# Kernel optimization log

Hardware: AMD Instinct MI355X
Metric: run time of the kernel (lower is better)

## Reference

```python
import jax, jax.numpy as jnp
import numpy as np

B, C, D, T = 64, 512, 32, 32
DT = D * T
K = 128            # valid_num: top-K proposals kept for NMS-style pooling
MARGIN = 0.2       # opt.global_margin
MAX_VIOLATION = True
EPS = 1e-8         # torch.cosine_similarity eps


def _l2n(x, axis):
    # torch cosine_similarity normalizes each vector by max(||x||, eps)
    return x / jnp.maximum(jnp.linalg.norm(x, axis=axis, keepdims=True), EPS)


def _cos(a, b, axis):
    return jnp.sum(_l2n(a, axis) * _l2n(b, axis), axis=axis)


def setup_inputs() -> dict:
    key = jax.random.key(0)
    k1, k2, k3 = jax.random.split(key, 3)
    videos = jax.random.normal(k1, (B, C, D, T), jnp.float32)
    sentences = jax.random.normal(k2, (B, C), jnp.float32)
    iou = jax.random.uniform(k3, (DT, DT), jnp.float32)
    iou_maps = 0.5 * (iou + iou.T)
    iou_maps = iou_maps.at[jnp.arange(DT), jnp.arange(DT)].set(1.0)
    mask = jnp.ones((D, T), jnp.float32)
    lam = jnp.asarray(0.125, jnp.float32)
    return {"videos": videos, "sentences": sentences, "lam": lam,
            "mask": mask, "valid_num": K, "iou_maps": iou_maps}


def reference(videos, sentences, lam, mask, valid_num, iou_maps):
    b, c, d, t = videos.shape
    dt = d * t
    # center over channel dim (dim=1 in torch)
    V = videos - jnp.mean(videos, axis=1, keepdims=True)          # [b,c,d,t]
    S = sentences - jnp.mean(sentences, axis=1, keepdims=True)    # [b,c]
    Vf = V.reshape(b, c, dt)
    Vn = _l2n(Vf, axis=1)                                         # unit over c
    Sn = _l2n(S, axis=1)
    mflat = mask.reshape(dt)

    # cosine sim of every sentence vs every video proposal: [b_sent, b_vid, dt]
    cross = jnp.einsum('ic,jcp->ijp', Sn, Vn)
    cross = jnp.where(mflat == 0, -jnp.inf, cross)

    # --- per-sample positive pooling (loop 1) ---
    self_score = cross[jnp.arange(b), jnp.arange(b)]              # [b, dt]
    w = jax.nn.softmax(self_score, axis=-1)
    video_pos = jnp.einsum('bp,bcp->bc', w, Vf)                   # [b, c]

    # sentence-sentence sims + hard negative mining
    sim = Sn @ Sn.T                                               # [b, b]
    idx = jnp.argsort(-sim, axis=1)                               # descending
    neg_idx = idx[:, 6:b - 5]                                     # b > 11 path
    neg_sents = S[neg_idx]                                        # [b, b-11, c]
    pos_score = _cos(video_pos, S, axis=1)                        # [b]
    neg_score = _cos(video_pos[:, None, :], neg_sents, axis=2)    # [b, b-11]
    vas_loss = jnp.mean(jax.nn.relu(MARGIN + neg_score - pos_score[:, None]), axis=1).mean()

    # cross-video pseudo-positive (crov), gated on nearest-neighbor sim > 0.9
    nn_idx = idx[:, 1]
    pse = Vf[nn_idx]                                              # [b, c, dt]
    vsim = jax.nn.softmax(_cos(video_pos[:, :, None], pse, axis=1), axis=-1)  # [b, dt]
    p_v = jnp.einsum('bp,bcp->bc', vsim, pse)
    n_v = jnp.einsum('bp,bcp->bc', (1.0 - vsim) * mflat, pse) / (valid_num - 1)
    crov = jax.nn.relu(MARGIN + _cos(video_pos, n_v, axis=1) - _cos(video_pos, p_v, axis=1))
    gate = sim[jnp.arange(b), nn_idx] > 0.9
    crov_loss = jnp.where(gate, crov, 0.0).mean()

    # --- NMS-weighted video score pooling (loop 2) ---
    pmap = self_score.reshape(b, d, t)                            # postive_map
    topv, topi = jax.lax.top_k(cross, valid_num)                  # [b,b,K]
    # pairwise IoU among the top-K proposals of each (sentence, video) pair
    iou = iou_maps[topi[..., :, None], topi[..., None, :]]        # [b,b,K,K]
    lower = jnp.tril(jnp.ones((valid_num, valid_num), bool), -1)  # l < k
    decay = jnp.prod(1.0 - jnp.where(lower, iou, 0.0), axis=-1)   # [b,b,K]
    wk = jax.nn.softmax(lam * topv, axis=-1)
    scores = jnp.sum(wk * decay * topv, axis=-1)                  # [b,b]

    # bidirectional margin ranking loss
    diag = jnp.diag(scores)[:, None]
    eye = jnp.eye(b, dtype=bool)
    cost_s = jnp.where(eye, 0.0, jax.nn.relu(MARGIN + scores - diag))
    cost_im = jnp.where(eye, 0.0, jax.nn.relu(MARGIN + scores - diag.T))
    if MAX_VIOLATION:
        cost_s = cost_s.max(axis=1)
        cost_im = cost_im.max(axis=0)
    loss = cost_s.sum() / b + cost_im.sum() / b + vas_loss + crov_loss
    return loss, pmap
```

## Files before the change

### kernel.cpp

```cpp
#include <hip/hip_runtime.h>
#include <hip/hip_fp16.h>
#include <math.h>

#define BB 64
#define CC 512
#define DTT 1024
#define NNEG 53
#define MARGIN_ 0.2f
#define EPSV 1e-8f
#define LDB 132

typedef short s16x8 __attribute__((ext_vector_type(8)));
typedef float f32x4 __attribute__((ext_vector_type(4)));

__device__ __forceinline__ float bred_sum(float v, float* red, int tid, int nt) {
  red[tid] = v; __syncthreads();
  for (int s = nt >> 1; s > 0; s >>= 1) { if (tid < s) red[tid] += red[tid + s]; __syncthreads(); }
  float r = red[0]; __syncthreads();
  return r;
}
__device__ __forceinline__ float bred_max(float v, float* red, int tid, int nt) {
  red[tid] = v; __syncthreads();
  for (int s = nt >> 1; s > 0; s >>= 1) { if (tid < s) red[tid] = fmaxf(red[tid], red[tid + s]); __syncthreads(); }
  float r = red[0]; __syncthreads();
  return r;
}

__global__ void k_sent(const float* __restrict__ sent, float* __restrict__ Sn,
                       float* __restrict__ SnT,
                       unsigned short* __restrict__ SnH, unsigned short* __restrict__ SnL,
                       float* __restrict__ SnSum) {
  int b = blockIdx.x, tid = threadIdx.x;
  __shared__ float red[256];
  float x0 = sent[b * CC + tid], x1 = sent[b * CC + tid + 256];
  float mean = bred_sum(x0 + x1, red, tid, 256) * (1.0f / CC);
  float s0 = x0 - mean, s1 = x1 - mean;
  float ss = bred_sum(s0 * s0 + s1 * s1, red, tid, 256);
  float nrm = fmaxf(sqrtf(ss), EPSV);
  float n0 = s0 / nrm, n1 = s1 / nrm;
  Sn[b * CC + tid] = n0; Sn[b * CC + tid + 256] = n1;
  SnT[tid * BB + b] = n0; SnT[(tid + 256) * BB + b] = n1;
  unsigned u0 = __float_as_uint(n0), u1 = __float_as_uint(n1);
  SnH[b * CC + tid] = (unsigned short)(u0 >> 16);
  SnH[b * CC + tid + 256] = (unsigned short)(u1 >> 16);
  float l0 = n0 - __uint_as_float(u0 & 0xFFFF0000u);
  float l1 = n1 - __uint_as_float(u1 & 0xFFFF0000u);
  SnL[b * CC + tid] = (unsigned short)(__float_as_uint(l0) >> 16);
  SnL[b * CC + tid + 256] = (unsigned short)(__float_as_uint(l1) >> 16);
  float sn = bred_sum(n0 + n1, red, tid, 256);
  if (tid == 0) SnSum[b] = sn;
}

__global__ void k_sim(const float* __restrict__ Sn, const float* __restrict__ SnT,
                      int* __restrict__ nn_idx, int* __restrict__ negidx,
                      float* __restrict__ nnsim) {
  int i = blockIdx.x, tid = threadIdx.x;
  int j = tid & 63, cq = tid >> 6;
  __shared__ float part[4][68];
  __shared__ float srow[BB];
  float acc = 0.f;
  const float* si = Sn + i * CC + cq * 128;
  const float* st = SnT + (size_t)(cq * 128) * BB + j;
#pragma unroll 8
  for (int c = 0; c < 128; ++c) acc = fmaf(si[c], st[(size_t)c * BB], acc);
  part[cq][j] = acc;
  __syncthreads();
  if (tid < 64) srow[tid] = part[0][tid] + part[1][tid] + part[2][tid] + part[3][tid];
  __syncthreads();
  if (tid < 64) {
    float mv = srow[tid];
    int rank = 0;
    for (int k = 0; k < BB; ++k) {
      float vk = srow[k];
      if (vk > mv || (vk == mv && k < tid)) rank++;
    }
    if (rank == 1) { nn_idx[i] = tid; nnsim[i] = mv; }
    if (rank >= 6 && rank < 59) negidx[i * NNEG + rank - 6] = tid;
  }
}

__global__ void k_prep_iou(const float* __restrict__ iou, __half* __restrict__ L16) {
  int g = (blockIdx.x * 256 + threadIdx.x) * 4;
  float4 x = *(const float4*)(iou + g);
  __half2 h0 = __floats2half2_rn(1.f - x.x, 1.f - x.y);
  __half2 h1 = __floats2half2_rn(1.f - x.z, 1.f - x.w);
  *(__half2*)(L16 + g) = h0;
  *(__half2*)(L16 + g + 2) = h1;
}

__global__ __launch_bounds__(256) void k_cross(const float* __restrict__ videos,
    const unsigned short* __restrict__ SnH, const unsigned short* __restrict__ SnL,
    const float* __restrict__ SnSum, const float* __restrict__ mask,
    float* __restrict__ cross, float* __restrict__ meanv, float* __restrict__ normv) {
  __shared__ unsigned int BH[2][16][LDB];
  __shared__ unsigned int BL[2][16][LDB];
  __shared__ float SnSum_s[64];
  __shared__ float mb_s[128];
  __shared__ float inv_s[128];

  int tid = threadIdx.x;
  int j = blockIdx.x >> 3;
  int p0 = (blockIdx.x & 7) << 7;
  int lane = tid & 63;
  int wv = tid >> 6;
  int row = lane & 15;
  int g = lane >> 4;
  int g8 = g << 3;
  int pA = wv << 5;

  int kp = tid >> 4;
  int pb = (tid & 15) << 3;

  const float* vbase = videos + ((size_t)j * CC) * DTT + p0;

  f32x4 acc[4][2];
#pragma unroll
  for (int a = 0; a < 4; ++a)
#pragma unroll
    for (int pf = 0; pf < 2; ++pf)
#pragma unroll
      for (int r = 0; r < 4; ++r) acc[a][pf][r] = 0.f;

  float sacc[8], ssacc[8];
#pragma unroll
  for (int q = 0; q < 8; ++q) { sacc[q] = 0.f; ssacc[q] = 0.f; }

  const float* pr = vbase + (size_t)(2 * kp) * DTT + pb;
  float4 f0 = *(const float4*)(pr);
  float4 f1 = *(const float4*)(pr + 4);
  float4 f2 = *(const float4*)(pr + DTT);
  float4 f3 = *(const float4*)(pr + DTT + 4);

#pragma unroll
  for (int t = 0; t < 16; ++t) {
    int kc = t * 32;
    int cb = t & 1;
    s16x8 AH[4], AL[4];
#pragma unroll
    for (int a = 0; a < 4; ++a) {
      int off = (a * 16 + row) * CC + kc + g8;
      AH[a] = *(const s16x8*)(SnH + off);
      AL[a] = *(const s16x8*)(SnL + off);
    }
    {
      float xe[8] = {f0.x, f0.y, f0.z, f0.w, f1.x, f1.y, f1.z, f1.w};
      float xo[8] = {f2.x, f2.y, f2.z, f2.w, f3.x, f3.y, f3.z, f3.w};
      unsigned int hw[8], lw[8];
#pragma unroll
      for (int q = 0; q < 8; ++q) {
        unsigned ue = __float_as_uint(xe[q]);
        unsigned uo = __float_as_uint(xo[q]);
        hw[q] = (ue >> 16) | (uo & 0xFFFF0000u);
        float el = xe[q] - __uint_as_float(ue & 0xFFFF0000u);
        float ol = xo[q] - __uint_as_float(uo & 0xFFFF0000u);
        lw[q] = (__float_as_uint(el) >> 16) | (__float_as_uint(ol) & 0xFFFF0000u);
        sacc[q] += xe[q] + xo[q];
        ssacc[q] = fmaf(xe[q], xe[q], ssacc[q]);
        ssacc[q] = fmaf(xo[q], xo[q], ssacc[q]);
      }
      *(uint4*)&BH[cb][kp][pb]     = make_uint4(hw[0], hw[1], hw[2], hw[3]);
      *(uint4*)&BH[cb][kp][pb + 4] = make_uint4(hw[4], hw[5], hw[6], hw[7]);
      *(uint4*)&BL[cb][kp][pb]     = make_uint4(lw[0], lw[1], lw[2], lw[3]);
      *(uint4*)&BL[cb][kp][pb + 4] = make_uint4(lw[4], lw[5], lw[6], lw[7]);
    }
    __syncthreads();
    if (t + 1 < 16) {
      const float* pn = vbase + (size_t)((t + 1) * 32 + 2 * kp) * DTT + pb;
      f0 = *(const float4*)(pn);
      f1 = *(const float4*)(pn + 4);
      f2 = *(const float4*)(pn + DTT);
      f3 = *(const float4*)(pn + DTT + 4);
    }
#pragma unroll
    for (int pf = 0; pf < 2; ++pf) {
      int p = pA + pf * 16 + row;
      int kpb = g << 2;
      union { unsigned int u[4]; s16x8 v; } bh, bl;
      bh.u[0] = BH[cb][kpb][p]; bh.u[1] = BH[cb][kpb + 1][p];
      bh.u[2] = BH[cb][kpb + 2][p]; bh.u[3] = BH[cb][kpb + 3][p];
      bl.u[0] = BL[cb][kpb][p]; bl.u[1] = BL[cb][kpb + 1][p];
      bl.u[2] = BL[cb][kpb + 2][p]; bl.u[3] = BL[cb][kpb + 3][p];
#pragma unroll
      for (int a = 0; a < 4; ++a) {
        acc[a][pf] = __builtin_amdgcn_mfma_f32_16x16x32_bf16(AH[a], bh.v, acc[a][pf], 0, 0, 0);
        acc[a][pf] = __builtin_amdgcn_mfma_f32_16x16x32_bf16(AH[a], bl.v, acc[a][pf], 0, 0, 0);
        acc[a][pf] = __builtin_amdgcn_mfma_f32_16x16x32_bf16(AL[a], bh.v, acc[a][pf], 0, 0, 0);
      }
    }
  }

  float (*Sred)[LDB] = (float(*)[LDB])&BH[0][0][0];
  float (*SSred)[LDB] = (float(*)[LDB])&BL[0][0][0];
#pragma unroll
  for (int q = 0; q < 8; ++q) { Sred[kp][pb + q] = sacc[q]; SSred[kp][pb + q] = ssacc[q]; }
  if (tid < 64) SnSum_s[tid] = SnSum[tid];
  __syncthreads();
  if (tid < 128) {
    float s = 0.f, ss = 0.f;
#pragma unroll
    for (int k = 0; k < 16; ++k) { s += Sred[k][tid]; ss += SSred[k][tid]; }
    float mb = s * (1.0f / CC);
    float var = ss - s * mb;
    float nrm = fmaxf(sqrtf(fmaxf(var, 0.f)), EPSV);
    meanv[j * DTT + p0 + tid] = mb;
    normv[j * DTT + p0 + tid] = nrm;
    mb_s[tid] = mb;
    inv_s[tid] = 1.f / nrm;
  }
  __syncthreads();

#pragma unroll
  for (int pf = 0; pf < 2; ++pf) {
    int p = pA + pf * 16 + row;
    float mb = mb_s[p], inv = inv_s[p];
    float mk = mask[p0 + p];
#pragma unroll
    for (int a = 0; a < 4; ++a) {
#pragma unroll
      for (int r = 0; r < 4; ++r) {
        int i = a * 16 + (g << 2) + r;
        float val = (acc[a][pf][r] - mb * SnSum_s[i]) * inv;
        if (mk == 0.f) val = -INFINITY;
        cross[((size_t)i * BB + j) * DTT + p0 + p] = val;
      }
    }
  }
}

__global__ void k_softmax_w(const float* __restrict__ cross, const float* __restrict__ meanv,
                            float* __restrict__ pmap, float* __restrict__ w, float* __restrict__ wm) {
  int b = blockIdx.x, tid = threadIdx.x;
  __shared__ float red[256];
  const float* row = cross + ((size_t)b * BB + b) * DTT;
  float v[4]; float mx = -INFINITY;
#pragma unroll
  for (int q = 0; q < 4; ++q) {
    v[q] = row[q * 256 + tid];
    pmap[b * DTT + q * 256 + tid] = v[q];
    mx = fmaxf(mx, v[q]);
  }
  mx = bred_max(mx, red, tid, 256);
  float e[4]; float se = 0.f;
#pragma unroll
  for (int q = 0; q < 4; ++q) { e[q] = expf(v[q] - mx); se += e[q]; }
  se = bred_sum(se, red, tid, 256);
  float inv = 1.f / se;
  float wmacc = 0.f;
#pragma unroll
  for (int q = 0; q < 4; ++q) {
    float wv = e[q] * inv;
    w[b * DTT + q * 256 + tid] = wv;
    wmacc += wv * meanv[b * DTT + q * 256 + tid];
  }
  wmacc = bred_sum(wmacc, red, tid, 256);
  if (tid == 0) wm[b] = wmacc;
}

__global__ void k_vpos(const float* __restrict__ videos, const float* __restrict__ w,
                       const float* __restrict__ wm, float* __restrict__ vp) {
  int wid = (blockIdx.x * 256 + threadIdx.x) >> 6;
  int lane = threadIdx.x & 63;
  int b = wid >> 9, c = wid & 511;
  const float4* vb = (const float4*)(videos + (size_t)(b * CC + c) * DTT) + lane * 4;
  const float4* wb = (const float4*)(w + b * DTT) + lane * 4;
  float acc = 0.f;
#pragma unroll
  for (int q = 0; q < 4; ++q) {
    float4 x = vb[q], y = wb[q];
    acc += x.x * y.x + x.y * y.y + x.z * y.z + x.w * y.w;
  }
#pragma unroll
  for (int off = 32; off > 0; off >>= 1) acc += __shfl_xor(acc, off);
  if (lane == 0) vp[b * CC + c] = acc - wm[b];
}

__global__ void k_vpnorm(const float* __restrict__ vp, float* __restrict__ vpn,
                         float* __restrict__ vpsum) {
  int b = blockIdx.x, tid = threadIdx.x;
  __shared__ float red[256];
  float x0 = vp[b * CC + tid], x1 = vp[b * CC + tid + 256];
  float ss = bred_sum(x0 * x0 + x1 * x1, red, tid, 256);
  float sm = bred_sum(x0 + x1, red, tid, 256);
  if (tid == 0) { vpn[b] = fmaxf(sqrtf(ss), EPSV); vpsum[b] = sm; }
}

__global__ void k_vsim_logits(const float* __restrict__ videos, const float* __restrict__ vp,
    const float* __restrict__ vpn, const float* __restrict__ vpsum, const int* __restrict__ nn_idx,
    const float* __restrict__ meanv, const float* __restrict__ normv, float* __restrict__ vslog) {
  int gid = blockIdx.x * 256 + threadIdx.x;
  int b = gid >> 10, p = gid & 1023;
  int nn = nn_idx[b];
  const float* base = videos + (size_t)nn * CC * DTT + p;
  const float* vpr = vp + b * CC;
  float acc = 0.f;
#pragma unroll 1
  for (int c0 = 0; c0 < CC; c0 += 16) {
    float v[16];
#pragma unroll
    for (int u = 0; u < 16; ++u) v[u] = base[(size_t)(c0 + u) * DTT];
#pragma unroll
    for (int u = 0; u < 16; ++u) acc = fmaf(vpr[c0 + u], v[u], acc);
  }
  acc -= meanv[nn * DTT + p] * vpsum[b];
  vslog[gid] = acc / (vpn[b] * normv[nn * DTT + p]);
}

__global__ void k_softmax_vsim(float* __restrict__ vslog, const int* __restrict__ nn_idx,
    const float* __restrict__ meanv, const float* __restrict__ mask,
    float* __restrict__ svp, float* __restrict__ svn) {
  int b = blockIdx.x, tid = threadIdx.x;
  __shared__ float red[256];
  int nn = nn_idx[b];
  float v[4]; float mx = -INFINITY;
#pragma unroll
  for (int q = 0; q < 4; ++q) { v[q] = vslog[b * DTT + q * 256 + tid]; mx = fmaxf(mx, v[q]); }
  mx = bred_max(mx, red, tid, 256);
  float e[4]; float se = 0.f;
#pragma unroll
  for (int q = 0; q < 4; ++q) { e[q] = expf(v[q] - mx); se += e[q]; }
  se = bred_sum(se, red, tid, 256);
  float inv = 1.f / se;
  float sp = 0.f, sn2 = 0.f;
#pragma unroll
  for (int q = 0; q < 4; ++q) {
    int p = q * 256 + tid;
    float vs = e[q] * inv;
    vslog[b * DTT + p] = vs;
    float mm = meanv[nn * DTT + p];
    sp += vs * mm;
    sn2 += (1.f - vs) * mask[p] * mm;
  }
  sp = bred_sum(sp, red, tid, 256);
  sn2 = bred_sum(sn2, red, tid, 256);
  if (tid == 0) { svp[b] = sp; svn[b] = sn2; }
}

__global__ void k_pvnv(const float* __restrict__ videos, const float* __restrict__ vsim,
    const int* __restrict__ nn_idx, const float* __restrict__ mask,
    const float* __restrict__ svp, const float* __restrict__ svn, const int* __restrict__ vn_p,
    float* __restrict__ pv, float* __restrict__ nv) {
  int wid = (blockIdx.x * 256 + threadIdx.x) >> 6;
  int lane = threadIdx.x & 63;
  int b = wid >> 9, c = wid & 511;
  int nn = nn_idx[b];
  const float4* vb = (const float4*)(videos + (size_t)(nn * CC + c) * DTT) + lane * 4;
  const float4* vs4 = (const float4*)(vsim + b * DTT) + lane * 4;
  const float4* m4 = ((const float4*)mask) + lane * 4;
  float ap = 0.f, an = 0.f;
#pragma unroll
  for (int q = 0; q < 4; ++q) {
    float4 x = vb[q], s = vs4[q], m = m4[q];
    ap += x.x * s.x + x.y * s.y + x.z * s.z + x.w * s.w;
    an += x.x * (1.f - s.x) * m.x + x.y * (1.f - s.y) * m.y + x.z * (1.f - s.z) * m.z + x.w * (1.f - s.w) * m.w;
  }
#pragma unroll
  for (int off = 32; off > 0; off >>= 1) { ap += __shfl_xor(ap, off); an += __shfl_xor(an, off); }
  if (lane == 0) {
    float kd = (float)(*vn_p - 1);
    pv[b * CC + c] = ap - svp[b];
    nv[b * CC + c] = (an - svn[b]) / kd;
  }
}

__global__ void k_vas(const float* __restrict__ vp, const float* __restrict__ vpn,
                      const float* __restrict__ SnT, const int* __restrict__ negidx,
                      float* __restrict__ vasrow) {
  int i = blockIdx.x, tid = threadIdx.x;
  int t = tid & 63, cq = tid >> 6;
  __shared__ float part[4][68];
  __shared__ float redv[64];
  __shared__ float red[256];
  int nj = (t < NNEG) ? negidx[i * NNEG + t] : i;
  float acc = 0.f;
  const float* vpr = vp + i * CC + cq * 128;
  const float* st = SnT + (size_t)(cq * 128) * BB + nj;
#pragma unroll 8
  for (int c = 0; c < 128; ++c) acc = fmaf(vpr[c], st[(size_t)c * BB], acc);
  part[cq][t] = acc;
  __syncthreads();
  if (tid < 64) redv[tid] = part[0][tid] + part[1][tid] + part[2][tid] + part[3][tid];
  __syncthreads();
  float invn = 1.f / vpn[i];
  float pos = redv[63] * invn;
  float contrib = (tid < NNEG) ? fmaxf(MARGIN_ + redv[tid] * invn - pos, 0.f) : 0.f;
  float s = bred_sum(contrib, red, tid, 256);
  if (tid == 0) vasrow[i] = s / (float)NNEG;
}

__global__ void k_crov(const float* __restrict__ vp, const float* __restrict__ vpn,
                       const float* __restrict__ pv, const float* __restrict__ nv,
                       const float* __restrict__ nnsim, float* __restrict__ crovrow) {
  int b = blockIdx.x, tid = threadIdx.x;
  __shared__ float red[256];
  float dp = 0.f, pp = 0.f, dn = 0.f, nn2 = 0.f;
  for (int c = tid; c < CC; c += 256) {
    float a = vp[b * CC + c], x = pv[b * CC + c], y = nv[b * CC + c];
    dp += a * x; pp += x * x; dn += a * y; nn2 += y * y;
  }
  dp = bred_sum(dp, red, tid, 256);
  pp = bred_sum(pp, red, tid, 256);
  dn = bred_sum(dn, red, tid, 256);
  nn2 = bred_sum(nn2, red, tid, 256);
  if (tid == 0) {
    float cosp = dp / (vpn[b] * fmaxf(sqrtf(pp), EPSV));
    float cosn = dn / (vpn[b] * fmaxf(sqrtf(nn2), EPSV));
    float crov = fmaxf(MARGIN_ + cosn - cosp, 0.f);
    crovrow[b] = (nnsim[b] > 0.9f) ? crov : 0.f;
  }
}

__global__ __launch_bounds__(256) void k_select(const float* __restrict__ cross,
    const int* __restrict__ vn_p, unsigned* __restrict__ ordi_g, float* __restrict__ ordv_g) {
  __shared__ unsigned int hist_s[4][256];
  __shared__ unsigned int sel_s[4][128];
  __shared__ unsigned int selk_s[4][128];
  __shared__ unsigned int cnt_s[4];
  int tid = threadIdx.x;
  int wv = tid >> 6, lane = tid & 63;
  int ij = blockIdx.x * 4 + wv;
  int K = *vn_p; if (K > 128) K = 128;
  unsigned int* hist = hist_s[wv];
  unsigned int* sel = sel_s[wv];
  unsigned int* selk = selk_s[wv];

  const float* row = cross + (size_t)ij * DTT;
  unsigned int v[16];
#pragma unroll
  for (int q = 0; q < 16; ++q) {
    unsigned u = __float_as_uint(row[q * 64 + lane]);
    v[q] = (u & 0x80000000u) ? ~u : (u | 0x80000000u);
  }
  if (lane == 0) cnt_s[wv] = 0u;
  __builtin_amdgcn_wave_barrier();

  unsigned prefix = 0u, pmask = 0u;
  int remaining = K;
  for (int shift = 24; shift >= 0; shift -= 8) {
#pragma unroll
    for (int q = 0; q < 4; ++q) hist[lane * 4 + q] = 0u;
    __builtin_amdgcn_wave_barrier();
#pragma unroll
    for (int q = 0; q < 16; ++q) {
      if ((v[q] & pmask) == prefix)
        atomicAdd(&hist[(v[q] >> shift) & 255u], 1u);
    }
    __builtin_amdgcn_wave_barrier();
    unsigned c0 = hist[lane * 4], c1 = hist[lane * 4 + 1];
    unsigned c2 = hist[lane * 4 + 2], c3 = hist[lane * 4 + 3];
    unsigned s = c0 + c1 + c2 + c3;
    unsigned inc = s;
#pragma unroll
    for (int off = 1; off < 64; off <<= 1) {
      unsigned t = __shfl_down(inc, off);
      if (lane + off < 64) inc += t;
    }
    unsigned exc = inc - s;
    bool found = (exc < (unsigned)remaining) && (inc >= (unsigned)remaining);
    unsigned long long bmask = __ballot(found);
    int winner = (int)(__ffsll((unsigned long long)bmask) - 1);
    unsigned packed = 0u;
    if (found) {
      unsigned c = exc;
      unsigned cc[4] = {c0, c1, c2, c3};
      int d = lane * 4;
#pragma unroll
      for (int q = 3; q >= 0; --q) {
        if (c + cc[q] >= (unsigned)remaining) { d = lane * 4 + q; break; }
        c += cc[q];
      }
      packed = ((unsigned)d << 16) | (unsigned)(remaining - (int)c);
    }
    packed = __shfl(packed, winner);
    prefix |= (packed >> 16) << shift;
    remaining = (int)(packed & 0xFFFFu);
    pmask |= 255u << shift;
  }

#pragma unroll
  for (int q = 0; q < 16; ++q) {
    if (v[q] > prefix) {
      unsigned pos = atomicAdd(&cnt_s[wv], 1u);
      sel[pos] = (unsigned)(q * 64 + lane);
      selk[pos] = v[q];
    }
  }
  __builtin_amdgcn_wave_barrier();
  {
    int base = K - remaining;
    int last = -1;
    for (int t = 0; t < remaining; ++t) {
      int mymin = 0x7FFFFFFF;
#pragma unroll
      for (int q = 0; q < 16; ++q) {
        int idx = q * 64 + lane;
        if (v[q] == prefix && idx > last && idx < mymin) mymin = idx;
      }
#pragma unroll
      for (int off = 32; off > 0; off >>= 1) mymin = min(mymin, __shfl_xor(mymin, off));
      if (lane == 0) { sel[base + t] = (unsigned)mymin; selk[base + t] = prefix; }
      last = mymin;
    }
  }
  __builtin_amdgcn_wave_barrier();

  for (int e = lane; e < K; e += 64) {
    unsigned myidx = sel[e], myk = selk[e];
    int rank = 0;
    for (int m = 0; m < K; ++m) {
      unsigned ok = selk[m];
      rank += (ok > myk || (ok == myk && sel[m] < myidx)) ? 1 : 0;
    }
    unsigned u = (myk & 0x80000000u) ? (myk & 0x7FFFFFFFu) : ~myk;
    ordi_g[ij * 128 + rank] = myidx;
    ordv_g[ij * 128 + rank] = __uint_as_float(u);
  }
}

__global__ __launch_bounds__(256) void k_decay(const __half* __restrict__ L16,
    const unsigned* __restrict__ ordi_g, const float* __restrict__ ordv_g,
    const float* __restrict__ lam_p, const int* __restrict__ vn_p,
    float* __restrict__ scores) {
  __shared__ unsigned ti[128];
  __shared__ float dks[128];
  int ij = blockIdx.x, tid = threadIdx.x;
  int wv = tid >> 6, lane = tid & 63;
  int K = *vn_p; if (K > 128) K = 128;
  float lam = *lam_p;
  if (tid < 128) {
    ti[tid] = (tid < K) ? ordi_g[ij * 128 + tid] : 0u;
    dks[tid] = 1.f;
  }
  __syncthreads();

  for (int r = wv; r < K; r += 4) {
    const __half* irow = L16 + (size_t)ti[r] * DTT;
    float f = 1.f;
    if (lane < r && lane < 64) f = __half2float(irow[ti[lane]]);
    float prod = f;
#pragma unroll
    for (int off = 32; off > 0; off >>= 1) prod *= __shfl_xor(prod, off);
    if (r > 64 && prod > 1e-14f) {
      float f2 = 1.f;
      int m = 64 + lane;
      if (m < r) f2 = __half2float(irow[ti[m]]);
#pragma unroll
      for (int off = 32; off > 0; off >>= 1) f2 *= __shfl_xor(f2, off);
      prod *= f2;
    }
    if (lane == 0) dks[r] = prod;
  }
  __syncthreads();

  if (wv == 0) {
    bool okA = (lane < K), okB = (lane + 64 < K);
    float vA = okA ? ordv_g[ij * 128 + lane] : 0.f;
    float vB = okB ? ordv_g[ij * 128 + lane + 64] : 0.f;
    float mx = fmaxf(okA ? lam * vA : -INFINITY, okB ? lam * vB : -INFINITY);
#pragma unroll
    for (int off = 32; off > 0; off >>= 1) mx = fmaxf(mx, __shfl_xor(mx, off));
    float eA = okA ? expf(lam * vA - mx) : 0.f;
    float eB = okB ? expf(lam * vB - mx) : 0.f;
    float se = eA + eB;
    float sc = (okA ? eA * dks[lane] * vA : 0.f) + (okB ? eB * dks[lane + 64] * vB : 0.f);
#pragma unroll
    for (int off = 32; off > 0; off >>= 1) {
      se += __shfl_xor(se, off);
      sc += __shfl_xor(sc, off);
    }
    if (lane == 0) scores[ij] = sc / se;
  }
}

__global__ void k_final(const float* __restrict__ scores, const float* __restrict__ vasrow,
                        const float* __restrict__ crovrow, float* __restrict__ out) {
  int tid = threadIdx.x;
  __shared__ float sm[BB * BB];
  __shared__ float red[64];
  for (int q = tid; q < BB * BB; q += 64) sm[q] = scores[q];
  __syncthreads();
  float di = sm[tid * BB + tid];
  float rowmax = 0.f, colmax = 0.f;
  for (int k = 0; k < BB; ++k) {
    if (k != tid) {
      rowmax = fmaxf(rowmax, fmaxf(MARGIN_ + sm[tid * BB + k] - di, 0.f));
      colmax = fmaxf(colmax, fmaxf(MARGIN_ + sm[k * BB + tid] - di, 0.f));
    }
  }
  float total = bred_sum(rowmax + colmax + vasrow[tid] + crovrow[tid], red, tid, 64);
  if (tid == 0) out[0] = total * (1.0f / BB);
}

extern "C" void kernel_launch(void* const* d_in, const int* in_sizes, int n_in,
                              void* d_out, int out_size, void* d_ws, size_t ws_size,
                              hipStream_t stream) {
  const float* videos = (const float*)d_in[0];
  const float* sentences = (const float*)d_in[1];
  const float* lam = (const float*)d_in[2];
  const float* mask = (const float*)d_in[3];
  const int* valid_num = (const int*)d_in[4];
  const float* iou_maps = (const float*)d_in[5];
  float* out = (float*)d_out;
  float* pmap = out + 1;

  float* ws = (float*)d_ws;
  float* Sn = ws;
  float* SnT = Sn + 32768;
  float* SnSum = SnT + 32768;
  float* meanv = SnSum + 64;
  float* normv = meanv + 65536;
  float* cross = normv + 65536;
  float* w = cross + 4194304;
  float* wm = w + 65536;
  float* vp = wm + 64;
  float* vpn = vp + 32768;
  float* vpsum = vpn + 64;
  float* nnsim = vpsum + 64;
  float* vslog = nnsim + 64;
  float* svp = vslog + 65536;
  float* svn = svp + 64;
  float* pvb = svn + 64;
  float* nvb = pvb + 32768;
  float* vasrow = nvb + 32768;
  float* crovrow = vasrow + 64;
  float* scores = crovrow + 64;
  int* nn_idx = (int*)(scores + 4096);
  int* negidx = nn_idx + 64;
  unsigned* ordi_g = (unsigned*)(negidx + 3392);
  float* ordv_g = (float*)(ordi_g + 524288);
  __half* L16 = (__half*)(ordv_g + 524288);
  unsigned short* SnH16 = (unsigned short*)(L16 + 1048576);
  unsigned short* SnL16 = SnH16 + 32768;

  k_sent<<<64, 256, 0, stream>>>(sentences, Sn, SnT, SnH16, SnL16, SnSum);
  k_sim<<<64, 256, 0, stream>>>(Sn, SnT, nn_idx, negidx, nnsim);
  k_prep_iou<<<1024, 256, 0, stream>>>(iou_maps, L16);
  k_cross<<<512, 256, 0, stream>>>(videos, SnH16, SnL16, SnSum, mask, cross, meanv, normv);
  k_softmax_w<<<64, 256, 0, stream>>>(cross, meanv, pmap, w, wm);
  k_vpos<<<8192, 256, 0, stream>>>(videos, w, wm, vp);
  k_vpnorm<<<64, 256, 0, stream>>>(vp, vpn, vpsum);
  k_vsim_logits<<<256, 256, 0, stream>>>(videos, vp, vpn, vpsum, nn_idx, meanv, normv, vslog);
  k_softmax_vsim<<<64, 256, 0, stream>>>(vslog, nn_idx, meanv, mask, svp, svn);
  k_pvnv<<<8192, 256, 0, stream>>>(videos, vslog, nn_idx, mask, svp, svn, valid_num, pvb, nvb);
  k_vas<<<64, 256, 0, stream>>>(vp, vpn, SnT, negidx, vasrow);
  k_crov<<<64, 256, 0, stream>>>(vp, vpn, pvb, nvb, nnsim, crovrow);
  k_select<<<1024, 256, 0, stream>>>(cross, valid_num, ordi_g, ordv_g);
  k_decay<<<4096, 256, 0, stream>>>(L16, ordi_g, ordv_g, lam, valid_num, scores);
  k_final<<<1, 64, 0, stream>>>(scores, vasrow, crovrow, out);
}
```

Before: 423.4 us.

## Restructure cross-sim kernel to single-wave blocks loading B fragments directly

The cross-similarity MFMA kernel moves from 256-thread blocks that stage split-bf16 video tiles through double-buffered LDS to 64-thread single-wave blocks, each covering 32 proposals. Each lane now loads its B-fragment values straight from global memory into registers, and column mean and sum-of-squares are reduced with cross-lane shuffles instead of LDS. This removes shared memory traffic and block barriers and raises the number of blocks from 512 to 2048. The cost is strided, less coalesced global loads (each lane reads 8 rows spaced DTT apart), no prefetch of the next chunk, and SnSum is read from global memory per lane.

New measurement: 435.8 us. 2.9% more time.

```diff
diff --git a/kernel.cpp b/kernel.cpp
--- a/kernel.cpp
+++ b/kernel.cpp
@@ -8,7 +8,6 @@
 #define NNEG 53
 #define MARGIN_ 0.2f
 #define EPSV 1e-8f
-#define LDB 132
 
 typedef short s16x8 __attribute__((ext_vector_type(8)));
 typedef float f32x4 __attribute__((ext_vector_type(4)));
@@ -88,30 +87,19 @@
   *(__half2*)(L16 + g + 2) = h1;
 }
 
-__global__ __launch_bounds__(256) void k_cross(const float* __restrict__ videos,
+__global__ __launch_bounds__(64) void k_cross(const float* __restrict__ videos,
     const unsigned short* __restrict__ SnH, const unsigned short* __restrict__ SnL,
     const float* __restrict__ SnSum, const float* __restrict__ mask,
     float* __restrict__ cross, float* __restrict__ meanv, float* __restrict__ normv) {
-  __shared__ unsigned int BH[2][16][LDB];
-  __shared__ unsigned int BL[2][16][LDB];
-  __shared__ float SnSum_s[64];
-  __shared__ float mb_s[128];
-  __shared__ float inv_s[128];
-
-  int tid = threadIdx.x;
-  int j = blockIdx.x >> 3;
-  int p0 = (blockIdx.x & 7) << 7;
-  int lane = tid & 63;
-  int wv = tid >> 6;
+  int lane = threadIdx.x;
+  int bid = blockIdx.x;
+  int j = bid >> 5;
+  int pbase = (bid & 31) << 5;
   int row = lane & 15;
   int g = lane >> 4;
   int g8 = g << 3;
-  int pA = wv << 5;
-
-  int kp = tid >> 4;
-  int pb = (tid & 15) << 3;
-
-  const float* vbase = videos + ((size_t)j * CC) * DTT + p0;
+
+  const float* vbase = videos + (size_t)j * CC * DTT;
 
   f32x4 acc[4][2];
 #pragma unroll
@@ -121,20 +109,11 @@
 #pragma unroll
       for (int r = 0; r < 4; ++r) acc[a][pf][r] = 0.f;
 
-  float sacc[8], ssacc[8];
-#pragma unroll
-  for (int q = 0; q < 8; ++q) { sacc[q] = 0.f; ssacc[q] = 0.f; }
-
-  const float* pr = vbase + (size_t)(2 * kp) * DTT + pb;
-  float4 f0 = *(const float4*)(pr);
-  float4 f1 = *(const float4*)(pr + 4);
-  float4 f2 = *(const float4*)(pr + DTT);
-  float4 f3 = *(const float4*)(pr + DTT + 4);
+  float sac[2] = {0.f, 0.f}, ssac[2] = {0.f, 0.f};
 
 #pragma unroll
   for (int t = 0; t < 16; ++t) {
     int kc = t * 32;
-    int cb = t & 1;
     s16x8 AH[4], AL[4];
 #pragma unroll
     for (int a = 0; a < 4; ++a) {
@@ -142,86 +121,68 @@
       AH[a] = *(const s16x8*)(SnH + off);
       AL[a] = *(const s16x8*)(SnL + off);
     }
-    {
-      float xe[8] = {f0.x, f0.y, f0.z, f0.w, f1.x, f1.y, f1.z, f1.w};
-      float xo[8] = {f2.x, f2.y, f2.z, f2.w, f3.x, f3.y, f3.z, f3.w};
-      unsigned int hw[8], lw[8];
-#pragma unroll
-      for (int q = 0; q < 8; ++q) {
-        unsigned ue = __float_as_uint(xe[q]);
-        unsigned uo = __float_as_uint(xo[q]);
+#pragma unroll
+    for (int pf = 0; pf < 2; ++pf) {
+      int p = pbase + pf * 16 + row;
+      const float* bp = vbase + (size_t)(kc + g8) * DTT + p;
+      float v[8];
+#pragma unroll
+      for (int q = 0; q < 8; ++q) v[q] = bp[(size_t)q * DTT];
+      unsigned int hw[4], lw[4];
+#pragma unroll
+      for (int q = 0; q < 4; ++q) {
+        float xe = v[2 * q], xo = v[2 * q + 1];
+        unsigned ue = __float_as_uint(xe);
+        unsigned uo = __float_as_uint(xo);
         hw[q] = (ue >> 16) | (uo & 0xFFFF0000u);
-        float el = xe[q] - __uint_as_float(ue & 0xFFFF0000u);
-        float ol = xo[q] - __uint_as_float(uo & 0xFFFF0000u);
+        float el = xe - __uint_as_float(ue & 0xFFFF0000u);
+        float ol = xo - __uint_as_float(uo & 0xFFFF0000u);
         lw[q] = (__float_as_uint(el) >> 16) | (__float_as_uint(ol) & 0xFFFF0000u);
-        sacc[q] += xe[q] + xo[q];
-        ssacc[q] = fmaf(xe[q], xe[q], ssacc[q]);
-        ssacc[q] = fmaf(xo[q], xo[q], ssacc[q]);
+        sac[pf] += xe + xo;
+        ssac[pf] = fmaf(xe, xe, ssac[pf]);
+        ssac[pf] = fmaf(xo, xo, ssac[pf]);
       }
-      *(uint4*)&BH[cb][kp][pb]     = make_uint4(hw[0], hw[1], hw[2], hw[3]);
-      *(uint4*)&BH[cb][kp][pb + 4] = make_uint4(hw[4], hw[5], hw[6], hw[7]);
-      *(uint4*)&BL[cb][kp][pb]     = make_uint4(lw[0], lw[1], lw[2], lw[3]);
-      *(uint4*)&BL[cb][kp][pb + 4] = make_uint4(lw[4], lw[5], lw[6], lw[7]);
-    }
-    __syncthreads();
-    if (t + 1 < 16) {
-      const float* pn = vbase + (size_t)((t + 1) * 32 + 2 * kp) * DTT + pb;
-      f0 = *(const float4*)(pn);
-      f1 = *(const float4*)(pn + 4);
-      f2 = *(const float4*)(pn + DTT);
-      f3 = *(const float4*)(pn + DTT + 4);
-    }
-#pragma unroll
-    for (int pf = 0; pf < 2; ++pf) {
-      int p = pA + pf * 16 + row;
-      int kpb = g << 2;
-      union { unsigned int u[4]; s16x8 v; } bh, bl;
-      bh.u[0] = BH[cb][kpb][p]; bh.u[1] = BH[cb][kpb + 1][p];
-      bh.u[2] = BH[cb][kpb + 2][p]; bh.u[3] = BH[cb][kpb + 3][p];
-      bl.u[0] = BL[cb][kpb][p]; bl.u[1] = BL[cb][kpb + 1][p];
-      bl.u[2] = BL[cb][kpb + 2][p]; bl.u[3] = BL[cb][kpb + 3][p];
+      union { unsigned int u[4]; s16x8 s; } bh, bl;
+      bh.u[0] = hw[0]; bh.u[1] = hw[1]; bh.u[2] = hw[2]; bh.u[3] = hw[3];
+      bl.u[0] = lw[0]; bl.u[1] = lw[1]; bl.u[2] = lw[2]; bl.u[3] = lw[3];
 #pragma unroll
       for (int a = 0; a < 4; ++a) {
-        acc[a][pf] = __builtin_amdgcn_mfma_f32_16x16x32_bf16(AH[a], bh.v, acc[a][pf], 0, 0, 0);
-        acc[a][pf] = __builtin_amdgcn_mfma_f32_16x16x32_bf16(AH[a], bl.v, acc[a][pf], 0, 0, 0);
-        acc[a][pf] = __builtin_amdgcn_mfma_f32_16x16x32_bf16(AL[a], bh.v, acc[a][pf], 0, 0, 0);
+        acc[a][pf] = __builtin_amdgcn_mfma_f32_16x16x32_bf16(AH[a], bh.s, acc[a][pf], 0, 0, 0);
+        acc[a][pf] = __builtin_amdgcn_mfma_f32_16x16x32_bf16(AH[a], bl.s, acc[a][pf], 0, 0, 0);
+        acc[a][pf] = __builtin_amdgcn_mfma_f32_16x16x32_bf16(AL[a], bh.s, acc[a][pf], 0, 0, 0);
       }
     }
   }
 
-  float (*Sred)[LDB] = (float(*)[LDB])&BH[0][0][0];
-  float (*SSred)[LDB] = (float(*)[LDB])&BL[0][0][0];
-#pragma unroll
-  for (int q = 0; q < 8; ++q) { Sred[kp][pb + q] = sacc[q]; SSred[kp][pb + q] = ssacc[q]; }
-  if (tid < 64) SnSum_s[tid] = SnSum[tid];
-  __syncthreads();
-  if (tid < 128) {
-    float s = 0.f, ss = 0.f;
-#pragma unroll
-    for (int k = 0; k < 16; ++k) { s += Sred[k][tid]; ss += SSred[k][tid]; }
+  float sns[16];
+#pragma unroll
+  for (int a = 0; a < 4; ++a)
+#pragma unroll
+    for (int r = 0; r < 4; ++r) sns[a * 4 + r] = SnSum[a * 16 + (g << 2) + r];
+
+#pragma unroll
+  for (int pf = 0; pf < 2; ++pf) {
+    float s = sac[pf], ss = ssac[pf];
+    s += __shfl_xor(s, 16); s += __shfl_xor(s, 32);
+    ss += __shfl_xor(ss, 16); ss += __shfl_xor(ss, 32);
+    int p = pbase + pf * 16 + row;
     float mb = s * (1.0f / CC);
     float var = ss - s * mb;
     float nrm = fmaxf(sqrtf(fmaxf(var, 0.f)), EPSV);
-    meanv[j * DTT + p0 + tid] = mb;
-    normv[j * DTT + p0 + tid] = nrm;
-    mb_s[tid] = mb;
-    inv_s[tid] = 1.f / nrm;
-  }
-  __syncthreads();
-
-#pragma unroll
-  for (int pf = 0; pf < 2; ++pf) {
-    int p = pA + pf * 16 + row;
-    float mb = mb_s[p], inv = inv_s[p];
-    float mk = mask[p0 + p];
+    float inv = 1.f / nrm;
+    if (g == 0) {
+      meanv[j * DTT + p] = mb;
+      normv[j * DTT + p] = nrm;
+    }
+    float mk = mask[p];
 #pragma unroll
     for (int a = 0; a < 4; ++a) {
 #pragma unroll
       for (int r = 0; r < 4; ++r) {
         int i = a * 16 + (g << 2) + r;
-        float val = (acc[a][pf][r] - mb * SnSum_s[i]) * inv;
+        float val = (acc[a][pf][r] - mb * sns[a * 4 + r]) * inv;
         if (mk == 0.f) val = -INFINITY;
-        cross[((size_t)i * BB + j) * DTT + p0 + p] = val;
+        cross[((size_t)i * BB + j) * DTT + p] = val;
       }
     }
   }
@@ -634,7 +595,7 @@
   k_sent<<<64, 256, 0, stream>>>(sentences, Sn, SnT, SnH16, SnL16, SnSum);
   k_sim<<<64, 256, 0, stream>>>(Sn, SnT, nn_idx, negidx, nnsim);
   k_prep_iou<<<1024, 256, 0, stream>>>(iou_maps, L16);
-  k_cross<<<512, 256, 0, stream>>>(videos, SnH16, SnL16, SnSum, mask, cross, meanv, normv);
+  k_cross<<<2048, 64, 0, stream>>>(videos, SnH16, SnL16, SnSum, mask, cross, meanv, normv);
   k_softmax_w<<<64, 256, 0, stream>>>(cross, meanv, pmap, w, wm);
   k_vpos<<<8192, 256, 0, stream>>>(videos, w, wm, vp);
   k_vpnorm<<<64, 256, 0, stream>>>(vp, vpn, vpsum);
```
